# Performance work log

Hardware: AMD Instinct MI355X
Metric: run time of the kernel (lower is better)

Reference implementation:

```python
import jax, jax.numpy as jnp
import numpy as np

EPS = 1.1920929e-07  # torch.finfo(float32).eps, used by F.rms_norm default

def rope(x, cos, sin):
    # x: [B,T,H,D]; cos/sin: [1,T,1,D//2]
    d = x.shape[-1] // 2
    x1, x2 = x[..., :d], x[..., d:]
    return jnp.concatenate([x1 * cos + x2 * sin, -x1 * sin + x2 * cos], axis=-1)

def rmsnorm(x):
    return x * jax.lax.rsqrt(jnp.mean(x * x, axis=-1, keepdims=True) + EPS)

def setup_inputs() -> dict:
    key = jax.random.key(0)
    ks = jax.random.split(key, 9)
    B, T, E = 2, 2048, 1024
    Hkv, D = 4, 64
    return {
        "x": jax.random.normal(ks[0], (B, T, E), jnp.float32),
        "ve": jax.random.normal(ks[1], (B, T, Hkv * D), jnp.float32),
        "cos": jax.random.normal(ks[2], (1, T, 1, D // 2), jnp.float32),
        "sin": jax.random.normal(ks[3], (1, T, 1, D // 2), jnp.float32),
        "Wq": jax.random.normal(ks[4], (E, E), jnp.float32) * 0.02,
        "Wk": jax.random.normal(ks[5], (Hkv * D, E), jnp.float32) * 0.02,
        "Wv": jax.random.normal(ks[6], (Hkv * D, E), jnp.float32) * 0.02,
        "Wproj": jax.random.normal(ks[7], (E, E), jnp.float32) * 0.02,
        "Wgate": jax.random.normal(ks[8], (Hkv, 32), jnp.float32) * 0.02,
        "window_size": 1024,
    }

def reference(x, ve, cos, sin, Wq, Wk, Wv, Wproj, Wgate, window_size):
    B, T, E = x.shape
    H, Hkv, D = 16, 4, 64
    G = H // Hkv  # GQA group size
    q = (x @ Wq.T).reshape(B, T, H, D)
    k = (x @ Wk.T).reshape(B, T, Hkv, D)
    v = (x @ Wv.T).reshape(B, T, Hkv, D)
    # value-embedding gating
    gate = 2.0 * jax.nn.sigmoid(x[..., :32] @ Wgate.T)          # [B,T,Hkv]
    v = v + gate[..., None] * ve.reshape(B, T, Hkv, D)
    # RoPE then QK RMS-norm
    q = rmsnorm(rope(q, cos, sin))
    k = rmsnorm(rope(k, cos, sin))
    # to [B,H,T,D]; repeat-interleave kv heads for GQA (matches torch enable_gqa)
    q = q.transpose(0, 2, 1, 3)
    k = jnp.repeat(k.transpose(0, 2, 1, 3), G, axis=1)
    v = jnp.repeat(v.transpose(0, 2, 1, 3), G, axis=1)
    # causal + sliding-window boolean mask
    row = jnp.arange(T)[:, None]
    col = jnp.arange(T)[None, :]
    mask = (col <= row) & (col >= row - window_size)            # [T,T]
    scale = 1.0 / jnp.sqrt(jnp.float32(D))
    scores = jnp.einsum("bhqd,bhkd->bhqk", q, k) * scale
    scores = jnp.where(mask, scores, -jnp.inf)
    p = jax.nn.softmax(scores, axis=-1)
    y = jnp.einsum("bhqk,bhkd->bhqd", p, v)
    y = y.transpose(0, 2, 1, 3).reshape(B, T, E)
    return y @ Wproj.T
```

## Files before the change

### kernel.cpp

```cpp
#include <hip/hip_runtime.h>


typedef float f32x4 __attribute__((ext_vector_type(4)));
typedef short s16x8 __attribute__((ext_vector_type(8)));
typedef short s16x4 __attribute__((ext_vector_type(4)));
typedef _Float16 f16x4 __attribute__((ext_vector_type(4)));

__device__ __forceinline__ unsigned short f2bf(float f) {
  unsigned u = __float_as_uint(f);
  u += 0x7fffu + ((u >> 16) & 1u);
  return (unsigned short)(u >> 16);
}

__device__ __forceinline__ float fexp2(float x) {
#if __has_builtin(__builtin_amdgcn_exp2f)
  return __builtin_amdgcn_exp2f(x);
#else
  return __expf(x * 0.69314718f);
#endif
}

__device__ __forceinline__ void gl2lds16(const unsigned short* g, unsigned short* l) {
  __builtin_amdgcn_global_load_lds((const __attribute__((address_space(1))) unsigned int*)g,
                                   (__attribute__((address_space(3))) unsigned int*)l, 16, 0, 0);
}

__global__ __launch_bounds__(256) void cvt_all(
    const float* __restrict__ x, const float* __restrict__ wq, const float* __restrict__ wk,
    const float* __restrict__ wv, const float* __restrict__ wp,
    unsigned short* __restrict__ xb, unsigned short* __restrict__ wqkv,
    unsigned short* __restrict__ wpj) {
  int i = blockIdx.x * 256 + threadIdx.x;
  const float* s;
  unsigned short* d;
  if (i < 1048576) { s = x; d = xb; }
  else if (i < 1310720) { i -= 1048576; s = wq; d = wqkv; }
  else if (i < 1376256) { i -= 1310720; s = wk; d = wqkv + 1048576; }
  else if (i < 1441792) { i -= 1376256; s = wv; d = wqkv + 1310720; }
  else { i -= 1441792; s = wp; d = wpj; }
  float4 v = ((const float4*)s)[i];
  ushort4 o;
  o.x = f2bf(v.x); o.y = f2bf(v.y); o.z = f2bf(v.z); o.w = f2bf(v.w);
  ((ushort4*)d)[i] = o;
}

__global__ __launch_bounds__(256) void gemm_bf16_64(
    const unsigned short* __restrict__ A, const unsigned short* __restrict__ B,
    float* __restrict__ C, int K, int ldc) {
  __shared__ unsigned short As[64 * 32];
  __shared__ unsigned short Bs[128 * 32];
  int bn = blockIdx.x, bm = blockIdx.y;
  int t = threadIdx.x;
  int w = t >> 6, lane = t & 63;
  int c = lane & 15, g = lane >> 4;
  int wm = w >> 1, wn = w & 1;

  f32x4 acc[2][4];
#pragma unroll
  for (int i = 0; i < 2; ++i)
#pragma unroll
    for (int j = 0; j < 4; ++j) acc[i][j] = (f32x4){0.f, 0.f, 0.f, 0.f};

  const unsigned short* Ab = A + (size_t)(bm * 64) * K;
  const unsigned short* Bb = B + (size_t)(bn * 128) * K;
  int srow = lane >> 2;
  int scol = (lane & 3) * 8;

  for (int k0 = 0; k0 < K; k0 += 32) {
    gl2lds16(Ab + (size_t)(w * 16 + srow) * K + k0 + scol, As + w * 512);
    gl2lds16(Bb + (size_t)(w * 16 + srow) * K + k0 + scol, Bs + w * 512);
    gl2lds16(Bb + (size_t)(64 + w * 16 + srow) * K + k0 + scol, Bs + 2048 + w * 512);
    __syncthreads();
    s16x8 af[2], bf[4];
#pragma unroll
    for (int mt = 0; mt < 2; ++mt)
      af[mt] = *(const s16x8*)(As + (wm * 32 + mt * 16 + c) * 32 + g * 8);
#pragma unroll
    for (int nt = 0; nt < 4; ++nt)
      bf[nt] = *(const s16x8*)(Bs + (wn * 64 + nt * 16 + c) * 32 + g * 8);
#pragma unroll
    for (int mt = 0; mt < 2; ++mt)
#pragma unroll
      for (int nt = 0; nt < 4; ++nt)
        acc[mt][nt] = __builtin_amdgcn_mfma_f32_16x16x32_bf16(af[mt], bf[nt], acc[mt][nt], 0, 0, 0);
    __syncthreads();
  }
#pragma unroll
  for (int mt = 0; mt < 2; ++mt)
#pragma unroll
    for (int nt = 0; nt < 4; ++nt)
#pragma unroll
      for (int r = 0; r < 4; ++r) {
        int rowg = bm * 64 + wm * 32 + mt * 16 + g * 4 + r;
        int colg = bn * 128 + wn * 64 + nt * 16 + c;
        C[(size_t)rowg * ldc + colg] = acc[mt][nt][r];
      }
}

__global__ __launch_bounds__(256) void post_qkv(
    const float* __restrict__ qkv, const float* __restrict__ x, const float* __restrict__ ve,
    const float* __restrict__ cosp, const float* __restrict__ sinp, const float* __restrict__ wgate,
    unsigned short* __restrict__ q_r, unsigned short* __restrict__ k_r,
    unsigned short* __restrict__ v_r) {
  int bt = blockIdx.x;
  int b = bt >> 11, t = bt & 2047;
  int w = threadIdx.x >> 6, lane = threadIdx.x & 63;
  const float* row = qkv + (size_t)bt * 1536;
  int dd = lane & 31;
  float cs = cosp[t * 32 + dd];
  float sn = sinp[t * 32 + dd];
  float sgn = (lane < 32) ? 1.f : -1.f;
  const float QSCL = 0.125f * 1.44269504f;

#pragma unroll
  for (int i = 0; i < 4; ++i) {
    int hh = w + i * 4;
    float val = row[hh * 64 + lane];
    float p = __shfl_xor(val, 32);
    float rr = val * cs + sgn * p * sn;
    float ss = rr * rr;
#pragma unroll
    for (int o = 32; o >= 1; o >>= 1) ss += __shfl_xor(ss, o);
    float sc = rsqrtf(ss * (1.0f / 64.0f) + 1.1920929e-07f);
    q_r[((size_t)(b * 16 + hh) * 2048 + t) * 64 + lane] = f2bf(rr * sc * QSCL);
  }
  {
    float val = row[1024 + w * 64 + lane];
    float p = __shfl_xor(val, 32);
    float rr = val * cs + sgn * p * sn;
    float ss = rr * rr;
#pragma unroll
    for (int o = 32; o >= 1; o >>= 1) ss += __shfl_xor(ss, o);
    float sc = rsqrtf(ss * (1.0f / 64.0f) + 1.1920929e-07f);
    k_r[((size_t)(b * 4 + w) * 2048 + t) * 64 + lane] = f2bf(rr * sc);
  }
  {
    float part = (lane < 32) ? x[(size_t)bt * 1024 + lane] * wgate[w * 32 + lane] : 0.f;
#pragma unroll
    for (int o = 32; o >= 1; o >>= 1) part += __shfl_xor(part, o);
    float gate = 2.f / (1.f + __expf(-part));
    float vv = row[1280 + w * 64 + lane] + gate * ve[(size_t)bt * 256 + w * 64 + lane];
    _Float16 hv = (_Float16)vv;
    v_r[((size_t)(b * 4 + w) * 2048 + t) * 64 + lane] = __builtin_bit_cast(unsigned short, hv);
  }
}

__global__ __launch_bounds__(256) void transpose_v(const unsigned short* __restrict__ v_r,
                                                   unsigned short* __restrict__ v_p2) {
  __shared__ unsigned short tile[64][72];
  int blk = blockIdx.x;
  int s = blk >> 5;
  int t0 = (blk & 31) * 64;
  int tt = threadIdx.x;
  int rcol = (tt & 7) * 8;
  int rrow = tt >> 3;
#pragma unroll
  for (int i = 0; i < 2; ++i) {
    int row = rrow + i * 32;
    *(s16x8*)&tile[row][rcol] = *(const s16x8*)(v_r + ((size_t)s * 2048 + t0 + row) * 64 + rcol);
  }
  __syncthreads();
#pragma unroll
  for (int i = 0; i < 2; ++i) {
    int idx = tt + i * 256;
    int ht = idx >> 8;
    int d = (idx >> 2) & 63;
    int e8 = (idx & 3) * 8;
    s16x8 o;
#pragma unroll
    for (int j = 0; j < 8; ++j) o[j] = tile[ht * 32 + e8 + j][d];
    *(s16x8*)(v_p2 + (size_t)s * 131072 + ((size_t)((t0 >> 5) + ht)) * 2048 + d * 32 + e8) = o;
  }
}

__global__ __launch_bounds__(256) void attn_kernel(
    const unsigned short* __restrict__ q_r, const unsigned short* __restrict__ k_r,
    const unsigned short* __restrict__ v_p2, unsigned short* __restrict__ y_b,
    const int* __restrict__ wptr) {
  const int W = *wptr;
  const int bid = blockIdx.x;
  const int qt = bid & 31, h = (bid >> 5) & 15, b = bid >> 9;
  const int tid = threadIdx.x;
  const int w = tid >> 6, lane = tid & 63, c = lane & 15, g = lane >> 4;
  const int r0b = qt * 64;
  const int r0w = r0b + w * 16;
  const int hkv = h >> 2;
  const float M = 11.5415603f;

  __shared__ unsigned short Ks[32 * 68];
  __shared__ unsigned short Vs[64 * 40];

  const unsigned short* kbase = k_r + (size_t)(b * 4 + hkv) * 131072;
  const unsigned short* vbase = v_p2 + (size_t)(b * 4 + hkv) * 131072;
  const unsigned short* qbase = q_r + ((size_t)(b * 16 + h) * 2048 + r0w) * 64;

  s16x8 q_lo = *(const s16x8*)(qbase + c * 64 + g * 8);
  s16x8 q_hi = *(const s16x8*)(qbase + c * 64 + 32 + g * 8);

  int kt0w = r0w - W; if (kt0w < 0) kt0w = 0;
  const int ktEw = r0w + 16;
  int KT0 = r0b - W; if (KT0 < 0) KT0 = 0;
  KT0 &= ~31;
  const int KTE = r0b + 64;

  float l_part = 0.f;
  f32x4 acc[4];
#pragma unroll
  for (int dt = 0; dt < 4; ++dt) acc[dt] = (f32x4){0.f, 0.f, 0.f, 0.f};

  s16x8 pk = *(const s16x8*)(kbase + (size_t)KT0 * 64 + tid * 8);
  s16x8 pv = *(const s16x8*)(vbase + (size_t)(KT0 >> 5) * 2048 + tid * 8);

  unsigned short* kdst = Ks + (tid >> 3) * 68 + (tid & 7) * 8;
  unsigned short* vdst = Vs + (tid >> 2) * 40 + (tid & 3) * 8;

  for (int kt = KT0; kt < KTE; kt += 32) {
    int nkt = (kt + 32 < KTE) ? kt + 32 : kt;
    s16x8 nk = *(const s16x8*)(kbase + (size_t)nkt * 64 + tid * 8);
    s16x8 nv = *(const s16x8*)(vbase + (size_t)(nkt >> 5) * 2048 + tid * 8);

    *(s16x4*)kdst = __builtin_shufflevector(pk, pk, 0, 1, 2, 3);
    *(s16x4*)(kdst + 4) = __builtin_shufflevector(pk, pk, 4, 5, 6, 7);
    *(s16x8*)vdst = pv;
    __syncthreads();

    if (kt + 32 > kt0w && kt < ktEw) {
      const unsigned short* kr0 = Ks + c * 68 + g * 8;
      s16x4 a0 = *(const s16x4*)(kr0);
      s16x4 a1 = *(const s16x4*)(kr0 + 4);
      s16x4 a2 = *(const s16x4*)(kr0 + 32);
      s16x4 a3 = *(const s16x4*)(kr0 + 36);
      const unsigned short* kr1 = kr0 + 16 * 68;
      s16x4 a4 = *(const s16x4*)(kr1);
      s16x4 a5 = *(const s16x4*)(kr1 + 4);
      s16x4 a6 = *(const s16x4*)(kr1 + 32);
      s16x4 a7 = *(const s16x4*)(kr1 + 36);
      s16x8 k0lo = __builtin_shufflevector(a0, a1, 0, 1, 2, 3, 4, 5, 6, 7);
      s16x8 k0hi = __builtin_shufflevector(a2, a3, 0, 1, 2, 3, 4, 5, 6, 7);
      s16x8 k1lo = __builtin_shufflevector(a4, a5, 0, 1, 2, 3, 4, 5, 6, 7);
      s16x8 k1hi = __builtin_shufflevector(a6, a7, 0, 1, 2, 3, 4, 5, 6, 7);

      f32x4 S0 = (f32x4){0.f, 0.f, 0.f, 0.f};
      f32x4 S1 = (f32x4){0.f, 0.f, 0.f, 0.f};
      S0 = __builtin_amdgcn_mfma_f32_16x16x32_bf16(k0lo, q_lo, S0, 0, 0, 0);
      S0 = __builtin_amdgcn_mfma_f32_16x16x32_bf16(k0hi, q_hi, S0, 0, 0, 0);
      S1 = __builtin_amdgcn_mfma_f32_16x16x32_bf16(k1lo, q_lo, S1, 0, 0, 0);
      S1 = __builtin_amdgcn_mfma_f32_16x16x32_bf16(k1hi, q_hi, S1, 0, 0, 0);

      f16x4 P0, P1;
      const bool edge = (kt < kt0w + 32) || (kt + 32 > r0w);
      const int qrow = r0w + c;
#pragma unroll
      for (int r = 0; r < 4; ++r) {
        float p0 = fexp2(S0[r] - M);
        float p1 = fexp2(S1[r] - M);
        if (edge) {
          int k0i = kt + g * 4 + r;
          int k1i = k0i + 16;
          if (!(k0i <= qrow && k0i >= qrow - W)) p0 = 0.f;
          if (!(k1i <= qrow && k1i >= qrow - W)) p1 = 0.f;
        }
        l_part += p0 + p1;
        P0[r] = (_Float16)p0;
        P1[r] = (_Float16)p1;
      }

#pragma unroll
      for (int dt = 0; dt < 4; ++dt) {
        const unsigned short* vr = Vs + (dt * 16 + c) * 40 + g * 4;
        f16x4 va = *(const f16x4*)(vr);
        f16x4 vb = *(const f16x4*)(vr + 16);
        acc[dt] = __builtin_amdgcn_mfma_f32_16x16x16f16(va, P0, acc[dt], 0, 0, 0);
        acc[dt] = __builtin_amdgcn_mfma_f32_16x16x16f16(vb, P1, acc[dt], 0, 0, 0);
      }
    }
    __syncthreads();
    pk = nk; pv = nv;
  }

  float l = l_part;
  l += __shfl_xor(l, 16);
  l += __shfl_xor(l, 32);
  float inv = 1.0f / l;

  unsigned short* ob = y_b + ((size_t)(b * 2048 + r0w + c) * 16 + h) * 64 + g * 4;
#pragma unroll
  for (int dt = 0; dt < 4; ++dt) {
    ushort4 o;
    o.x = f2bf(acc[dt][0] * inv);
    o.y = f2bf(acc[dt][1] * inv);
    o.z = f2bf(acc[dt][2] * inv);
    o.w = f2bf(acc[dt][3] * inv);
    *(ushort4*)(ob + dt * 16) = o;
  }
}

extern "C" void kernel_launch(void* const* d_in, const int* in_sizes, int n_in,
                              void* d_out, int out_size, void* d_ws, size_t ws_size,
                              hipStream_t stream) {
  const float* x = (const float*)d_in[0];
  const float* ve = (const float*)d_in[1];
  const float* cosp = (const float*)d_in[2];
  const float* sinp = (const float*)d_in[3];
  const float* Wq = (const float*)d_in[4];
  const float* Wk = (const float*)d_in[5];
  const float* Wv = (const float*)d_in[6];
  const float* Wproj = (const float*)d_in[7];
  const float* Wgate = (const float*)d_in[8];
  const int* wptr = (const int*)d_in[9];

  unsigned short* xb = (unsigned short*)d_ws;
  unsigned short* wqkv = xb + 4194304;
  unsigned short* wpj = wqkv + 1572864;
  unsigned short* q_r = wpj + 1048576;
  unsigned short* k_r = q_r + 4194304;
  unsigned short* v_r = k_r + 1048576;
  unsigned short* y_b = v_r + 1048576;
  float* qkv = (float*)(y_b + 4194304);
  unsigned short* vp2 = (unsigned short*)qkv;

  cvt_all<<<6656, 256, 0, stream>>>(x, Wq, Wk, Wv, Wproj, xb, wqkv, wpj);
  gemm_bf16_64<<<dim3(12, 64), 256, 0, stream>>>(xb, wqkv, qkv, 1024, 1536);
  post_qkv<<<4096, 256, 0, stream>>>(qkv, x, ve, cosp, sinp, Wgate, q_r, k_r, v_r);
  transpose_v<<<256, 256, 0, stream>>>(v_r, vp2);
  attn_kernel<<<1024, 256, 0, stream>>>(q_r, k_r, vp2, y_b, wptr);
  gemm_bf16_64<<<dim3(8, 64), 256, 0, stream>>>(y_b, wpj, (float*)d_out, 1024, 1024);
}
```

Measured before the change: 192.4 us.

## Fuse RoPE, RMS-norm and value gating into QKV GEMM epilogue

The QKV projection GEMM now applies RoPE, QK RMS-norm, scaling and value-embedding gating in its epilogue and writes bf16/fp16 q, k, v directly. This removes the fp32 qkv intermediate round-trip and the separate post-processing kernel. The gate sigmoid moves to a small standalone kernel, and the GEMM tile grows to 128x128 with fewer blocks, which raises register pressure and lowers the block count. The epilogue writes are scattered 2-byte stores.

```diff
diff --git a/kernel.cpp b/kernel.cpp
--- a/kernel.cpp
+++ b/kernel.cpp
@@ -10,6 +10,10 @@
   unsigned u = __float_as_uint(f);
   u += 0x7fffu + ((u >> 16) & 1u);
   return (unsigned short)(u >> 16);
+}
+__device__ __forceinline__ unsigned short h16(float f) {
+  _Float16 h = (_Float16)f;
+  return __builtin_bit_cast(unsigned short, h);
 }
 
 __device__ __forceinline__ float fexp2(float x) {
@@ -44,6 +48,122 @@
   ((ushort4*)d)[i] = o;
 }
 
+__global__ __launch_bounds__(256) void gate_kernel(const float* __restrict__ x,
+                                                   const float* __restrict__ wgate,
+                                                   float* __restrict__ gatep) {
+  int i = blockIdx.x * 256 + threadIdx.x;
+  int bt = i >> 2, h = i & 3;
+  const float4* xp = (const float4*)(x + (size_t)bt * 1024);
+  const float4* wp = (const float4*)(wgate + h * 32);
+  float s = 0.f;
+#pragma unroll
+  for (int j = 0; j < 8; ++j) {
+    float4 a = xp[j], b = wp[j];
+    s += a.x * b.x + a.y * b.y + a.z * b.z + a.w * b.w;
+  }
+  gatep[i] = 2.f / (1.f + __expf(-s));
+}
+
+__global__ __launch_bounds__(256) void gemm_qkv(
+    const unsigned short* __restrict__ A, const unsigned short* __restrict__ B,
+    const float* __restrict__ cosp, const float* __restrict__ sinp,
+    const float* __restrict__ gatep, const float* __restrict__ ve,
+    unsigned short* __restrict__ q_r, unsigned short* __restrict__ k_r,
+    unsigned short* __restrict__ v_r) {
+  __shared__ unsigned short As[128 * 32];
+  __shared__ unsigned short Bs[128 * 32];
+  const int K = 1024;
+  int bn = blockIdx.x, bm = blockIdx.y;
+  int t = threadIdx.x;
+  int w = t >> 6, lane = t & 63;
+  int c = lane & 15, g = lane >> 4;
+  int wm = w >> 1, wn = w & 1;
+
+  f32x4 acc[4][4];
+#pragma unroll
+  for (int i = 0; i < 4; ++i)
+#pragma unroll
+    for (int j = 0; j < 4; ++j) acc[i][j] = (f32x4){0.f, 0.f, 0.f, 0.f};
+
+  const unsigned short* Ab = A + (size_t)(bm * 128) * K;
+  const unsigned short* Bb = B + (size_t)(bn * 128) * K;
+  int srow = lane >> 2;
+  int scol = (lane & 3) * 8;
+
+  for (int k0 = 0; k0 < K; k0 += 32) {
+#pragma unroll
+    for (int j = 0; j < 2; ++j) {
+      int rbase = j * 64 + w * 16;
+      gl2lds16(Ab + (size_t)(rbase + srow) * K + k0 + scol, As + rbase * 32);
+      gl2lds16(Bb + (size_t)(rbase + srow) * K + k0 + scol, Bs + rbase * 32);
+    }
+    __syncthreads();
+    s16x8 af[4], bf[4];
+#pragma unroll
+    for (int mt = 0; mt < 4; ++mt)
+      af[mt] = *(const s16x8*)(As + (wm * 64 + mt * 16 + c) * 32 + g * 8);
+#pragma unroll
+    for (int nt = 0; nt < 4; ++nt)
+      bf[nt] = *(const s16x8*)(Bs + (wn * 64 + nt * 16 + c) * 32 + g * 8);
+#pragma unroll
+    for (int mt = 0; mt < 4; ++mt)
+#pragma unroll
+      for (int nt = 0; nt < 4; ++nt)
+        acc[mt][nt] = __builtin_amdgcn_mfma_f32_16x16x32_bf16(af[mt], bf[nt], acc[mt][nt], 0, 0, 0);
+    __syncthreads();
+  }
+
+  const float QSCL = 0.125f * 1.44269504f;
+#pragma unroll
+  for (int mt = 0; mt < 4; ++mt) {
+#pragma unroll
+    for (int r = 0; r < 4; ++r) {
+      int row = bm * 128 + wm * 64 + mt * 16 + g * 4 + r;
+      int b = row >> 11, tt = row & 2047;
+      float v0 = acc[mt][0][r], v1 = acc[mt][1][r], v2 = acc[mt][2][r], v3 = acc[mt][3][r];
+      if (bn < 10) {
+        float cs0 = cosp[tt * 32 + c], sn0 = sinp[tt * 32 + c];
+        float cs1 = cosp[tt * 32 + 16 + c], sn1 = sinp[tt * 32 + 16 + c];
+        float r0 = v0 * cs0 + v2 * sn0;
+        float r1 = v1 * cs1 + v3 * sn1;
+        float r2 = v2 * cs0 - v0 * sn0;
+        float r3 = v3 * cs1 - v1 * sn1;
+        float ss = r0 * r0 + r1 * r1 + r2 * r2 + r3 * r3;
+        ss += __shfl_xor(ss, 1);
+        ss += __shfl_xor(ss, 2);
+        ss += __shfl_xor(ss, 4);
+        ss += __shfl_xor(ss, 8);
+        float sc = rsqrtf(ss * (1.0f / 64.0f) + 1.1920929e-07f);
+        if (bn < 8) {
+          int h = bn * 2 + wn;
+          unsigned short* qp = q_r + ((size_t)(b * 16 + h) * 2048 + tt) * 64;
+          float s2 = sc * QSCL;
+          qp[c] = f2bf(r0 * s2);
+          qp[16 + c] = f2bf(r1 * s2);
+          qp[32 + c] = f2bf(r2 * s2);
+          qp[48 + c] = f2bf(r3 * s2);
+        } else {
+          int h = (bn - 8) * 2 + wn;
+          unsigned short* kp = k_r + ((size_t)(b * 4 + h) * 2048 + tt) * 64;
+          kp[c] = f2bf(r0 * sc);
+          kp[16 + c] = f2bf(r1 * sc);
+          kp[32 + c] = f2bf(r2 * sc);
+          kp[48 + c] = f2bf(r3 * sc);
+        }
+      } else {
+        int h = (bn - 10) * 2 + wn;
+        float gate = gatep[row * 4 + h];
+        const float* vep = ve + (size_t)row * 256 + h * 64;
+        unsigned short* vp = v_r + ((size_t)(b * 4 + h) * 2048 + tt) * 64;
+        vp[c] = h16(v0 + gate * vep[c]);
+        vp[16 + c] = h16(v1 + gate * vep[16 + c]);
+        vp[32 + c] = h16(v2 + gate * vep[32 + c]);
+        vp[48 + c] = h16(v3 + gate * vep[48 + c]);
+      }
+    }
+  }
+}
+
 __global__ __launch_bounds__(256) void gemm_bf16_64(
     const unsigned short* __restrict__ A, const unsigned short* __restrict__ B,
     float* __restrict__ C, int K, int ldc) {
@@ -95,54 +215,6 @@
         int colg = bn * 128 + wn * 64 + nt * 16 + c;
         C[(size_t)rowg * ldc + colg] = acc[mt][nt][r];
       }
-}
-
-__global__ __launch_bounds__(256) void post_qkv(
-    const float* __restrict__ qkv, const float* __restrict__ x, const float* __restrict__ ve,
-    const float* __restrict__ cosp, const float* __restrict__ sinp, const float* __restrict__ wgate,
-    unsigned short* __restrict__ q_r, unsigned short* __restrict__ k_r,
-    unsigned short* __restrict__ v_r) {
-  int bt = blockIdx.x;
-  int b = bt >> 11, t = bt & 2047;
-  int w = threadIdx.x >> 6, lane = threadIdx.x & 63;
-  const float* row = qkv + (size_t)bt * 1536;
-  int dd = lane & 31;
-  float cs = cosp[t * 32 + dd];
-  float sn = sinp[t * 32 + dd];
-  float sgn = (lane < 32) ? 1.f : -1.f;
-  const float QSCL = 0.125f * 1.44269504f;
-
-#pragma unroll
-  for (int i = 0; i < 4; ++i) {
-    int hh = w + i * 4;
-    float val = row[hh * 64 + lane];
-    float p = __shfl_xor(val, 32);
-    float rr = val * cs + sgn * p * sn;
-    float ss = rr * rr;
-#pragma unroll
-    for (int o = 32; o >= 1; o >>= 1) ss += __shfl_xor(ss, o);
-    float sc = rsqrtf(ss * (1.0f / 64.0f) + 1.1920929e-07f);
-    q_r[((size_t)(b * 16 + hh) * 2048 + t) * 64 + lane] = f2bf(rr * sc * QSCL);
-  }
-  {
-    float val = row[1024 + w * 64 + lane];
-    float p = __shfl_xor(val, 32);
-    float rr = val * cs + sgn * p * sn;
-    float ss = rr * rr;
-#pragma unroll
-    for (int o = 32; o >= 1; o >>= 1) ss += __shfl_xor(ss, o);
-    float sc = rsqrtf(ss * (1.0f / 64.0f) + 1.1920929e-07f);
-    k_r[((size_t)(b * 4 + w) * 2048 + t) * 64 + lane] = f2bf(rr * sc);
-  }
-  {
-    float part = (lane < 32) ? x[(size_t)bt * 1024 + lane] * wgate[w * 32 + lane] : 0.f;
-#pragma unroll
-    for (int o = 32; o >= 1; o >>= 1) part += __shfl_xor(part, o);
-    float gate = 2.f / (1.f + __expf(-part));
-    float vv = row[1280 + w * 64 + lane] + gate * ve[(size_t)bt * 256 + w * 64 + lane];
-    _Float16 hv = (_Float16)vv;
-    v_r[((size_t)(b * 4 + w) * 2048 + t) * 64 + lane] = __builtin_bit_cast(unsigned short, hv);
-  }
 }
 
 __global__ __launch_bounds__(256) void transpose_v(const unsigned short* __restrict__ v_r,
@@ -316,12 +388,12 @@
   unsigned short* k_r = q_r + 4194304;
   unsigned short* v_r = k_r + 1048576;
   unsigned short* y_b = v_r + 1048576;
-  float* qkv = (float*)(y_b + 4194304);
-  unsigned short* vp2 = (unsigned short*)qkv;
+  unsigned short* vp2 = y_b + 4194304;
+  float* gatep = (float*)(vp2 + 1048576);
 
   cvt_all<<<6656, 256, 0, stream>>>(x, Wq, Wk, Wv, Wproj, xb, wqkv, wpj);
-  gemm_bf16_64<<<dim3(12, 64), 256, 0, stream>>>(xb, wqkv, qkv, 1024, 1536);
-  post_qkv<<<4096, 256, 0, stream>>>(qkv, x, ve, cosp, sinp, Wgate, q_r, k_r, v_r);
+  gate_kernel<<<64, 256, 0, stream>>>(x, Wgate, gatep);
+  gemm_qkv<<<dim3(12, 32), 256, 0, stream>>>(xb, wqkv, cosp, sinp, gatep, ve, q_r, k_r, v_r);
   transpose_v<<<256, 256, 0, stream>>>(v_r, vp2);
   attn_kernel<<<1024, 256, 0, stream>>>(q_r, k_r, vp2, y_b, wptr);
   gemm_bf16_64<<<dim3(8, 64), 256, 0, stream>>>(y_b, wpj, (float*)d_out, 1024, 1024);
```

Result: no change. 191.8 us (-0.3%).
